# Kernel tuning notes

Measured on AMD Instinct MI355X. Metric: run time of the kernel, lower is better.

Reference implementation:

```python
import jax, jax.numpy as jnp
import numpy as np

L, H, HD, D, FF, V, S_LEN = 12, 12, 64, 768, 3072, 50257, 1024
NEG = jnp.finfo(jnp.float32).min


def _ln(x, g, b, eps=1e-5):
    mu = x.mean(-1, keepdims=True)
    var = ((x - mu) ** 2).mean(-1, keepdims=True)
    return (x - mu) * jax.lax.rsqrt(var + eps) * g + b


def setup_inputs() -> dict:
    key = jax.random.key(0)
    ks = jax.random.split(key, 14)
    n = lambda k, shp, s=0.02: jax.random.normal(k, shp, jnp.float32) * s
    return {
        "input_ids": jax.random.randint(ks[0], (1, S_LEN), 0, V, dtype=jnp.int32),
        "attention_mask": jnp.ones((1, S_LEN), jnp.int32),
        "wte": n(ks[1], (V, D)),
        "wpe": n(ks[2], (S_LEN, D)),
        "ln1_g": 1.0 + n(ks[3], (L, D), 0.01),
        "ln1_b": n(ks[4], (L, D), 0.01),
        "W_qkv": n(ks[5], (L, D, 3 * D)),
        "b_qkv": n(ks[6], (L, 3 * D)),
        "W_o": n(ks[7], (L, D, D)),
        "b_o": n(ks[8], (L, D)),
        "ln2_g": 1.0 + n(ks[9], (L, D), 0.01),
        "ln2_b": n(ks[10], (L, D), 0.01),
        "W_fc": n(ks[11], (L, D, FF)),
        "b_fc": n(ks[12], (L, FF)),
        "W_proj": n(ks[13], (L, FF, D)),
        "b_proj": jnp.zeros((L, D), jnp.float32),
        "S": 20, "Sa1": 21, "S2": 600,
    }


def reference(input_ids, attention_mask, wte, wpe, ln1_g, ln1_b, W_qkv, b_qkv,
              W_o, b_o, ln2_g, ln2_b, W_fc, b_fc, W_proj, b_proj, S, Sa1, S2):
    T = input_ids.shape[-1]
    h0 = wte[input_ids[0]] + wpe[:T]                      # [T, D]
    causal = jnp.tril(jnp.ones((T, T), bool))
    add_mask = (1.0 - attention_mask[0].astype(jnp.float32)) * NEG  # [T]
    scale = 1.0 / np.sqrt(HD).astype(np.float32)

    def step(h, p):
        (l1g, l1b, Wqkv, bqkv, Wo, bo, l2g, l2b, Wfc, bfc, Wp, bp) = p
        xl = _ln(h, l1g, l1b)                             # pre-block LN, [T, D]
        # ---- standard GPT-2 block forward (advances hidden state) ----
        qkv = xl @ Wqkv + bqkv
        q, k, v = jnp.split(qkv, 3, axis=-1)
        q = q.reshape(T, H, HD).transpose(1, 0, 2)        # [H, T, HD]
        k = k.reshape(T, H, HD).transpose(1, 0, 2)
        v = v.reshape(T, H, HD).transpose(1, 0, 2)
        sc = jnp.einsum('hqd,hkd->hqk', q, k) * scale
        sc = jnp.where(causal, sc, NEG) + add_mask
        ctx = jnp.einsum('hqk,hkd->hqd', jax.nn.softmax(sc, axis=-1), v)
        attn_out = ctx.transpose(1, 0, 2).reshape(T, D) @ Wo + bo
        h2 = h + attn_out
        h_new = h2 + (jax.nn.gelu(_ln(h2, l2g, l2b) @ Wfc + bfc,
                                  approximate=True) @ Wp + bp)
        # ---- manual QK circuit decomposition (pre-block hidden state) ----
        Wq, Wk, _ = jnp.split(Wqkv, 3, axis=1)            # [D, D] each
        bq, bk, _ = jnp.split(bqkv, 3, axis=0)            # [D] each
        Wmhq = Wq.reshape(D, H, HD).transpose(1, 0, 2)    # [H, D, HD]
        Wmhk = Wk.reshape(D, H, HD).transpose(1, 0, 2)
        bqh = bq.reshape(H, HD)                           # [H, HD]
        bkh = bk.reshape(H, HD)
        qc = jnp.einsum('td,hdk->htk', xl, Wmhq)          # x W_q per head
        kc = jnp.einsum('td,hdk->htk', xl, Wmhk)          # x W_k per head
        term1 = jnp.einsum('hqk,htk->hqt', qc, kc)                 # x Wq Wk^T x^T
        term2 = jnp.einsum('hk,htk->ht', bqh, kc)[:, None, :]      # bq Wk^T x^T
        term3 = jnp.einsum('hqk,hk->hq', qc, bkh)[:, :, None]      # x Wq bk^T
        term4 = jnp.einsum('hk,hk->h', bqh, bkh)[:, None, None]    # bq bk^T
        scores = (term1 + term2 + term3 + term4) * scale
        aw = jax.nn.softmax(jnp.where(causal, scores, NEG), axis=-1)  # [H, T, T]
        dup = aw[:, S2, S]
        ind = aw[:, S2, Sa1]
        prev = aw[:, -1, S2]
        return h_new, (dup, ind, prev, prev)

    params = (ln1_g, ln1_b, W_qkv, b_qkv, W_o, b_o,
              ln2_g, ln2_b, W_fc, b_fc, W_proj, b_proj)
    _, (dup, ind, prev, name) = jax.lax.scan(step, h0, params)
    return dup, ind, prev, name   # each [L, H] = [12, 12]
```

## Files before the change

kernel.cpp:

```cpp
#include <hip/hip_runtime.h>
#include <hip/hip_bf16.h>
#include <math.h>

namespace {

constexpr int T = 1024;
constexpr int D = 768;
constexpr int FF = 3072;
constexpr int H = 12;
constexpr int HD = 64;
constexpr int L = 12;
constexpr float SCALE = 0.125f;

typedef __attribute__((ext_vector_type(8))) short short8;
typedef __attribute__((ext_vector_type(4))) float floatx4;

__device__ inline unsigned short f2bf(float f) {
    __hip_bfloat16 h = __float2bfloat16(f);
    return *reinterpret_cast<unsigned short*>(&h);
}
__device__ inline float bf2f(unsigned short u) {
    union { unsigned int i; float f; } c;
    c.i = (unsigned int)u << 16;
    return c.f;
}

__global__ void embed_kernel(const int* __restrict__ ids,
                             const float* __restrict__ wte,
                             const float* __restrict__ wpe,
                             float* __restrict__ h) {
    int i = blockIdx.x * blockDim.x + threadIdx.x;
    if (i >= T * D) return;
    int t = i / D, d = i % D;
    h[i] = wte[(long)ids[t] * D + d] + wpe[i];
}

__global__ __launch_bounds__(256)
void ln_kernel(const float* __restrict__ x, const float* __restrict__ g,
               const float* __restrict__ b, unsigned short* __restrict__ out) {
    int row = blockIdx.x, tid = threadIdx.x;
    const float* xr = x + (long)row * D;
    float v0 = xr[tid], v1 = xr[tid + 256], v2 = xr[tid + 512];
    __shared__ float red[4];
    __shared__ float share;
    float s = v0 + v1 + v2;
#pragma unroll
    for (int o = 32; o; o >>= 1) s += __shfl_down(s, o, 64);
    if ((tid & 63) == 0) red[tid >> 6] = s;
    __syncthreads();
    if (tid == 0) share = (red[0] + red[1] + red[2] + red[3]) * (1.0f / D);
    __syncthreads();
    float mu = share;
    float d0 = v0 - mu, d1 = v1 - mu, d2 = v2 - mu;
    float q = d0 * d0 + d1 * d1 + d2 * d2;
#pragma unroll
    for (int o = 32; o; o >>= 1) q += __shfl_down(q, o, 64);
    __syncthreads();
    if ((tid & 63) == 0) red[tid >> 6] = q;
    __syncthreads();
    if (tid == 0) share = rsqrtf((red[0] + red[1] + red[2] + red[3]) * (1.0f / D) + 1e-5f);
    __syncthreads();
    float rs = share;
    unsigned short* orow = out + (long)row * D;
    orow[tid]       = f2bf(d0 * rs * g[tid]       + b[tid]);
    orow[tid + 256] = f2bf(d1 * rs * g[tid + 256] + b[tid + 256]);
    orow[tid + 512] = f2bf(d2 * rs * g[tid + 512] + b[tid + 512]);
}

__global__ __launch_bounds__(256)
void wconvert_b(const float* __restrict__ W, unsigned short* __restrict__ WT,
                int K, int N) {
    const int zl = blockIdx.z;
    W  += (long)zl * K * N;
    WT += (long)zl * N * K;
    __shared__ float t[32][33];
    const int n0 = blockIdx.x * 32, k0 = blockIdx.y * 32;
    const int tx = threadIdx.x, ty = threadIdx.y;
#pragma unroll
    for (int i = 0; i < 4; i++)
        t[ty * 4 + i][tx] = W[(long)(k0 + ty * 4 + i) * N + n0 + tx];
    __syncthreads();
#pragma unroll
    for (int i = 0; i < 4; i++)
        WT[(long)(n0 + ty * 4 + i) * K + k0 + tx] = f2bf(t[tx][ty * 4 + i]);
}

#define GEMM_CORE(KLEN)                                                                 \
    floatx4 acc[2][4] = {};                                                             \
    {                                                                                   \
        *(short8*)&As[0][ablk][sl][0]     = *(const short8*)(ApA);                      \
        *(short8*)&As[0][ablk + 4][sl][0] = *(const short8*)(ApB);                      \
        *(short8*)&Bs[0][ablk][sl][0]     = *(const short8*)(Bp);                       \
    }                                                                                   \
    __syncthreads();                                                                    \
    const int nsteps = (KLEN) >> 5;                                                     \
    for (int s = 0; s < nsteps; s++) {                                                  \
        const int buf = s & 1;                                                          \
        short8 na0, na1, nbv;                                                           \
        const bool has_next = (s + 1 < nsteps);                                         \
        if (has_next) {                                                                 \
            na0 = *(const short8*)(ApA + (s + 1) * 32);                                 \
            na1 = *(const short8*)(ApB + (s + 1) * 32);                                 \
            nbv = *(const short8*)(Bp + (s + 1) * 32);                                  \
        }                                                                               \
        short8 af[2], bfr[4];                                                           \
        _Pragma("unroll")                                                               \
        for (int mi = 0; mi < 2; mi++)                                                  \
            af[mi] = *(const short8*)&As[buf][w * 2 + mi][lane][0];                     \
        _Pragma("unroll")                                                               \
        for (int ni = 0; ni < 4; ni++)                                                  \
            bfr[ni] = *(const short8*)&Bs[buf][ni][lane][0];                            \
        _Pragma("unroll")                                                               \
        for (int mi = 0; mi < 2; mi++)                                                  \
            _Pragma("unroll")                                                           \
            for (int ni = 0; ni < 4; ni++)                                              \
                acc[mi][ni] = __builtin_amdgcn_mfma_f32_16x16x32_bf16(                  \
                    af[mi], bfr[ni], acc[mi][ni], 0, 0, 0);                             \
        if (has_next) {                                                                 \
            const int nb = buf ^ 1;                                                     \
            *(short8*)&As[nb][ablk][sl][0]     = na0;                                   \
            *(short8*)&As[nb][ablk + 4][sl][0] = na1;                                   \
            *(short8*)&Bs[nb][ablk][sl][0]     = nbv;                                   \
        }                                                                               \
        __syncthreads();                                                                \
    }

#define GEMM_PRELUDE(KOFF)                                                              \
    const int tid = threadIdx.x;                                                        \
    const int w = tid >> 6, lane = tid & 63;                                            \
    const int ablk = tid >> 6;                                                          \
    const int sl = tid & 63;                                                            \
    const int row0 = blockIdx.y * 128, col0 = blockIdx.x * 64;                          \
    __shared__ unsigned short As[2][8][64][8];                                          \
    __shared__ unsigned short Bs[2][4][64][8];                                          \
    const unsigned short* ApA = A + (long)(row0 + ablk * 16 + (sl & 15)) * K + (KOFF) + (sl >> 4) * 8; \
    const unsigned short* ApB = ApA + 64L * K;                                          \
    const unsigned short* Bp  = BT + (long)(col0 + ablk * 16 + (sl & 15)) * K + (KOFF) + (sl >> 4) * 8;

__global__ __launch_bounds__(256)
void gemm_fused(const unsigned short* __restrict__ A, const unsigned short* __restrict__ BT,
                const float* __restrict__ bias, unsigned short* __restrict__ Cb,
                int N, int K, int flags) {
    GEMM_PRELUDE(0)
    GEMM_CORE(K)
#pragma unroll
    for (int mi = 0; mi < 2; mi++) {
        int rg = row0 + (w * 2 + mi) * 16 + (lane >> 4) * 4;
#pragma unroll
        for (int ni = 0; ni < 4; ni++) {
            int cg = col0 + ni * 16 + (lane & 15);
            float bv = (flags & 1) ? bias[cg] : 0.f;
            float bscale = ((flags & 16) && cg < D) ? SCALE : 1.0f;
#pragma unroll
            for (int r = 0; r < 4; r++) {
                float v = acc[mi][ni][r] + bv;
                if (flags & 4) {
                    float zz = 0.7978845608028654f * (v + 0.044715f * v * v * v);
                    v = v / (1.0f + __expf(-2.0f * zz));
                }
                Cb[(long)(rg + r) * N + cg] = f2bf(v * bscale);
            }
        }
    }
}

__global__ __launch_bounds__(256)
void gemm_bf16(const unsigned short* __restrict__ A, const unsigned short* __restrict__ BT,
               float* __restrict__ part, int N, int K, int splitK) {
    const int z = blockIdx.z;
    const int Kc = K / splitK;
    GEMM_PRELUDE(z * Kc)
    GEMM_CORE(Kc)
    float* dst = part + (long)z * T * N;
#pragma unroll
    for (int mi = 0; mi < 2; mi++) {
        int rg = row0 + (w * 2 + mi) * 16 + (lane >> 4) * 4;
#pragma unroll
        for (int ni = 0; ni < 4; ni++) {
            int cg = col0 + ni * 16 + (lane & 15);
#pragma unroll
            for (int r = 0; r < 4; r++)
                dst[(long)(rg + r) * N + cg] = acc[mi][ni][r];
        }
    }
}

__global__ __launch_bounds__(256)
void reduce_ln(const float* __restrict__ part, const float* __restrict__ bias,
               const float* __restrict__ resid,
               const float* __restrict__ g, const float* __restrict__ b,
               float* __restrict__ Cres, unsigned short* __restrict__ Cln,
               int splitK) {
    const int row = blockIdx.x, tid = threadIdx.x;
    const int c0 = tid, c1 = tid + 256, c2 = tid + 512;
    const long rb = (long)row * D;
    float v0 = bias[c0] + resid[rb + c0];
    float v1 = bias[c1] + resid[rb + c1];
    float v2 = bias[c2] + resid[rb + c2];
    for (int z = 0; z < splitK; z++) {
        const float* p = part + (long)z * T * D + rb;
        v0 += p[c0]; v1 += p[c1]; v2 += p[c2];
    }
    float* crow = Cres + rb;
    crow[c0] = v0; crow[c1] = v1; crow[c2] = v2;
    __shared__ float red[4];
    __shared__ float share;
    float s = v0 + v1 + v2;
#pragma unroll
    for (int o = 32; o; o >>= 1) s += __shfl_down(s, o, 64);
    if ((tid & 63) == 0) red[tid >> 6] = s;
    __syncthreads();
    if (tid == 0) share = (red[0] + red[1] + red[2] + red[3]) * (1.0f / D);
    __syncthreads();
    float mu = share;
    float d0 = v0 - mu, d1 = v1 - mu, d2 = v2 - mu;
    float q = d0 * d0 + d1 * d1 + d2 * d2;
#pragma unroll
    for (int o = 32; o; o >>= 1) q += __shfl_down(q, o, 64);
    __syncthreads();
    if ((tid & 63) == 0) red[tid >> 6] = q;
    __syncthreads();
    if (tid == 0) share = rsqrtf((red[0] + red[1] + red[2] + red[3]) * (1.0f / D) + 1e-5f);
    __syncthreads();
    float rs = share;
    unsigned short* orow = Cln + rb;
    orow[c0] = f2bf(d0 * rs * g[c0] + b[c0]);
    orow[c1] = f2bf(d1 * rs * g[c1] + b[c1]);
    orow[c2] = f2bf(d2 * rs * g[c2] + b[c2]);
}

__global__ __launch_bounds__(256)
void flash_mfma(const unsigned short* __restrict__ qkvb, unsigned short* __restrict__ ctxb) {
    const int h = blockIdx.y;
    const int q0 = blockIdx.x * 64;
    const int tid = threadIdx.x;
    const int w = tid >> 6;
    const int l = tid & 63;
    const int lm = l & 15;
    const int g = l >> 4;

    __shared__ unsigned short Kl[64][72];
    __shared__ unsigned short Vt[64][80];
    __shared__ unsigned short Pl[4][16][72];

    short8 qf[2];
    {
        const unsigned short* qp = qkvb + (long)(q0 + w * 16 + lm) * (3 * D) + h * HD + g * 8;
        qf[0] = *(const short8*)(qp);
        qf[1] = *(const short8*)(qp + 32);
    }

    const int d8 = (tid & 7) * 8;
    const int kp = (tid >> 3) * 2;

    float m = -INFINITY, lsum = 0.f;
    floatx4 o[4] = {};
    const int qw = q0 + w * 16;
    const int nt = blockIdx.x + 1;

    for (int t = 0; t < nt; t++) {
        const int c0 = t * 64;
        __syncthreads();
        {
            const unsigned short* kr0 = qkvb + (long)(c0 + kp) * (3 * D) + D + h * HD + d8;
            const unsigned short* kr1 = kr0 + 3 * D;
            *(short8*)&Kl[kp][d8]     = *(const short8*)kr0;
            *(short8*)&Kl[kp + 1][d8] = *(const short8*)kr1;
            short8 va = *(const short8*)(kr0 + D);
            short8 vb = *(const short8*)(kr1 + D);
#pragma unroll
            for (int j = 0; j < 8; j++) {
                unsigned int pk = (unsigned)(unsigned short)va[j] |
                                  ((unsigned)(unsigned short)vb[j] << 16);
                *(unsigned int*)&Vt[d8 + j][kp] = pk;
            }
        }
        __syncthreads();

        if (c0 > qw + 15) continue;

        floatx4 st[4] = {};
#pragma unroll
        for (int ks = 0; ks < 2; ks++)
#pragma unroll
            for (int mt = 0; mt < 4; mt++) {
                short8 af = *(const short8*)&Kl[mt * 16 + lm][ks * 32 + g * 8];
                st[mt] = __builtin_amdgcn_mfma_f32_16x16x32_bf16(af, qf[ks], st[mt], 0, 0, 0);
            }

        const int qg = qw + lm;
        if (c0 + 63 > qw) {
#pragma unroll
            for (int mt = 0; mt < 4; mt++)
#pragma unroll
                for (int r = 0; r < 4; r++)
                    if (c0 + mt * 16 + g * 4 + r > qg) st[mt][r] = -INFINITY;
        }
        float tmax = -INFINITY;
#pragma unroll
        for (int mt = 0; mt < 4; mt++)
#pragma unroll
            for (int r = 0; r < 4; r++) tmax = fmaxf(tmax, st[mt][r]);
        tmax = fmaxf(tmax, __shfl_xor(tmax, 16));
        tmax = fmaxf(tmax, __shfl_xor(tmax, 32));
        float mn = fmaxf(m, tmax);
        float alpha = __expf(m - mn);
        float psum = 0.f;
        unsigned short pb[16];
#pragma unroll
        for (int mt = 0; mt < 4; mt++)
#pragma unroll
            for (int r = 0; r < 4; r++) {
                float p = __expf(st[mt][r] - mn);
                psum += p;
                pb[mt * 4 + r] = f2bf(p);
            }
        lsum = lsum * alpha + psum;
        m = mn;
#pragma unroll
        for (int mt = 0; mt < 4; mt++) {
            unsigned int p0 = (unsigned)pb[mt * 4 + 0] | ((unsigned)pb[mt * 4 + 1] << 16);
            unsigned int p1 = (unsigned)pb[mt * 4 + 2] | ((unsigned)pb[mt * 4 + 3] << 16);
            *(unsigned int*)&Pl[w][lm][mt * 16 + g * 4]     = p0;
            *(unsigned int*)&Pl[w][lm][mt * 16 + g * 4 + 2] = p1;
        }
        float ar0 = __shfl(alpha, g * 4 + 0), ar1 = __shfl(alpha, g * 4 + 1);
        float ar2 = __shfl(alpha, g * 4 + 2), ar3 = __shfl(alpha, g * 4 + 3);
#pragma unroll
        for (int fd = 0; fd < 4; fd++) {
            o[fd][0] *= ar0; o[fd][1] *= ar1; o[fd][2] *= ar2; o[fd][3] *= ar3;
        }
#pragma unroll
        for (int ks = 0; ks < 2; ks++) {
            short8 pa = *(const short8*)&Pl[w][lm][ks * 32 + g * 8];
#pragma unroll
            for (int fd = 0; fd < 4; fd++) {
                short8 vb = *(const short8*)&Vt[fd * 16 + lm][ks * 32 + g * 8];
                o[fd] = __builtin_amdgcn_mfma_f32_16x16x32_bf16(pa, vb, o[fd], 0, 0, 0);
            }
        }
    }
    float l2 = lsum + __shfl_xor(lsum, 16);
    float l4 = l2 + __shfl_xor(l2, 32);
    float linv = 1.0f / l4;
    float lr0 = __shfl(linv, g * 4 + 0), lr1 = __shfl(linv, g * 4 + 1);
    float lr2 = __shfl(linv, g * 4 + 2), lr3 = __shfl(linv, g * 4 + 3);
#pragma unroll
    for (int fd = 0; fd < 4; fd++) {
        unsigned short* cp = ctxb + (long)(qw + g * 4) * D + h * HD + fd * 16 + lm;
        cp[0 * D] = f2bf(o[fd][0] * lr0);
        cp[1 * D] = f2bf(o[fd][1] * lr1);
        cp[2 * D] = f2bf(o[fd][2] * lr2);
        cp[3 * D] = f2bf(o[fd][3] * lr3);
    }
}

__global__ __launch_bounds__(256)
void probe_kernel(const unsigned short* __restrict__ qkvb,
                  const int* __restrict__ Sp, const int* __restrict__ Sa1p,
                  const int* __restrict__ S2p,
                  float* __restrict__ out, int layer) {
    const int h = blockIdx.y;
    const int which = blockIdx.x;
    const int s = *Sp, sa1 = *Sa1p, s2 = *S2p;
    const int row = which ? (T - 1) : s2;
    const int tid = threadIdx.x;
    __shared__ float qrow[64];
    __shared__ float prob[T];
    __shared__ float red[4];
    __shared__ float bshare;
    if (tid < 64) qrow[tid] = bf2f(qkvb[(long)row * (3 * D) + h * HD + tid]);
    __syncthreads();
    float mloc = -INFINITY;
    for (int j = tid; j <= row; j += 256) {
        const unsigned short* krow = qkvb + (long)j * (3 * D) + D + h * HD;
        float acc = 0;
#pragma unroll
        for (int d = 0; d < 64; d += 8) {
            short8 kv = *(const short8*)(krow + d);
#pragma unroll
            for (int e = 0; e < 8; e++)
                acc += qrow[d + e] * bf2f((unsigned short)kv[e]);
        }
        prob[j] = acc;
        mloc = fmaxf(mloc, acc);
    }
#pragma unroll
    for (int o = 32; o; o >>= 1) mloc = fmaxf(mloc, __shfl_down(mloc, o, 64));
    if ((tid & 63) == 0) red[tid >> 6] = mloc;
    __syncthreads();
    if (tid == 0) bshare = fmaxf(fmaxf(red[0], red[1]), fmaxf(red[2], red[3]));
    __syncthreads();
    float m = bshare;
    float ssum = 0;
    for (int j = tid; j <= row; j += 256) {
        float e = expf(prob[j] - m);
        prob[j] = e;
        ssum += e;
    }
#pragma unroll
    for (int o = 32; o; o >>= 1) ssum += __shfl_down(ssum, o, 64);
    __syncthreads();
    if ((tid & 63) == 0) red[tid >> 6] = ssum;
    __syncthreads();
    if (tid == 0) bshare = red[0] + red[1] + red[2] + red[3];
    __syncthreads();
    float inv = 1.0f / bshare;
    if (tid == 0) {
        if (which == 0) {
            out[0 * (L * H) + layer * H + h] = prob[s] * inv;
            out[1 * (L * H) + layer * H + h] = prob[sa1] * inv;
        } else {
            out[2 * (L * H) + layer * H + h] = prob[s2] * inv;
            out[3 * (L * H) + layer * H + h] = prob[s2] * inv;
        }
    }
}

}

extern "C" void kernel_launch(void* const* d_in, const int* in_sizes, int n_in,
                              void* d_out, int out_size, void* d_ws, size_t ws_size,
                              hipStream_t stream) {
    const int*   ids    = (const int*)  d_in[0];
    const float* wte    = (const float*)d_in[2];
    const float* wpe    = (const float*)d_in[3];
    const float* ln1_g  = (const float*)d_in[4];
    const float* ln1_b  = (const float*)d_in[5];
    const float* W_qkv  = (const float*)d_in[6];
    const float* b_qkv  = (const float*)d_in[7];
    const float* W_o    = (const float*)d_in[8];
    const float* b_o    = (const float*)d_in[9];
    const float* ln2_g  = (const float*)d_in[10];
    const float* ln2_b  = (const float*)d_in[11];
    const float* W_fc   = (const float*)d_in[12];
    const float* b_fc   = (const float*)d_in[13];
    const float* W_proj = (const float*)d_in[14];
    const float* b_proj = (const float*)d_in[15];
    const int*   Sp     = (const int*)  d_in[16];
    const int*   Sa1p   = (const int*)  d_in[17];
    const int*   S2p    = (const int*)  d_in[18];
    float* out = (float*)d_out;

    float* ws   = (float*)d_ws;
    float* h    = ws;
    float* h2   = h   + (long)T * D;
    float* part = h2  + (long)T * D;
    unsigned short* xl   = (unsigned short*)(part + 4L * T * D);
    unsigned short* qkvb = xl   + (long)T * D;
    unsigned short* ctxb = qkvb + (long)T * 3 * D;
    unsigned short* fb   = ctxb + (long)T * D;
    unsigned short* wt_qkv  = fb      + (long)T * FF;
    unsigned short* wt_o    = wt_qkv  + (long)L * 3 * D * D;
    unsigned short* wt_fc   = wt_o    + (long)L * D * D;
    unsigned short* wt_proj = wt_fc   + (long)L * D * FF;

    embed_kernel<<<(T * D + 255) / 256, 256, 0, stream>>>(ids, wte, wpe, h);
    wconvert_b<<<dim3(3 * D / 32, D / 32, L), dim3(32, 8), 0, stream>>>(W_qkv, wt_qkv, D, 3 * D);
    wconvert_b<<<dim3(D / 32, D / 32, L), dim3(32, 8), 0, stream>>>(W_o, wt_o, D, D);
    wconvert_b<<<dim3(FF / 32, D / 32, L), dim3(32, 8), 0, stream>>>(W_fc, wt_fc, D, FF);
    wconvert_b<<<dim3(D / 32, FF / 32, L), dim3(32, 8), 0, stream>>>(W_proj, wt_proj, FF, D);
    ln_kernel<<<T, 256, 0, stream>>>(h, ln1_g, ln1_b, xl);

    for (int l = 0; l < L; l++) {
        gemm_fused<<<dim3(3 * D / 64, T / 128), 256, 0, stream>>>(
            xl, wt_qkv + (long)l * 3 * D * D, b_qkv + (long)l * 3 * D,
            qkvb, 3 * D, D, 1 | 16);
        probe_kernel<<<dim3(2, H), 256, 0, stream>>>(qkvb, Sp, Sa1p, S2p, out, l);

        if (l == L - 1) break;

        flash_mfma<<<dim3(T / 64, H), 256, 0, stream>>>(qkvb, ctxb);
        gemm_bf16<<<dim3(D / 64, T / 128, 4), 256, 0, stream>>>(
            ctxb, wt_o + (long)l * D * D, part, D, D, 4);
        reduce_ln<<<T, 256, 0, stream>>>(
            part, b_o + (long)l * D, h, ln2_g + l * D, ln2_b + l * D, h2, xl, 4);
        gemm_fused<<<dim3(FF / 64, T / 128), 256, 0, stream>>>(
            xl, wt_fc + (long)l * D * FF, b_fc + (long)l * FF, fb, FF, D, 1 | 4);
        gemm_bf16<<<dim3(D / 64, T / 128, 4), 256, 0, stream>>>(
            fb, wt_proj + (long)l * D * FF, part, D, FF, 4);
        reduce_ln<<<T, 256, 0, stream>>>(
            part, b_proj + (long)l * D, h2, ln1_g + (l + 1) * D, ln1_b + (l + 1) * D, h, xl, 4);
    }
}
```

Baseline: 1.421 ms.

## Split flash attention across two key halves and use direct global-to-LDS GEMM loads

The flash attention kernel now splits each query tile's key range into two halves along a new grid z dimension. Each half writes unnormalized fp32 partial outputs plus its running max and sum, and a new merge kernel combines them into bf16 context. This doubles the block count so the GPU's compute units stay busier, at the cost of an extra kernel launch and extra fp32 traffic. Separately, the GEMM core now loads tiles with global_load_lds, which writes straight into LDS instead of staging through registers. That should cut register pressure and VGPR-to-LDS store instructions.

```diff
diff --git a/kernel.cpp b/kernel.cpp
--- a/kernel.cpp
+++ b/kernel.cpp
@@ -23,6 +23,11 @@
     union { unsigned int i; float f; } c;
     c.i = (unsigned int)u << 16;
     return c.f;
+}
+__device__ inline void gld16(const void* g, void* l) {
+    __builtin_amdgcn_global_load_lds(
+        (const __attribute__((address_space(1))) void*)g,
+        (__attribute__((address_space(3))) void*)l, 16, 0, 0);
 }
 
 __global__ void embed_kernel(const int* __restrict__ ids,
@@ -87,21 +92,18 @@
 
 #define GEMM_CORE(KLEN)                                                                 \
     floatx4 acc[2][4] = {};                                                             \
-    {                                                                                   \
-        *(short8*)&As[0][ablk][sl][0]     = *(const short8*)(ApA);                      \
-        *(short8*)&As[0][ablk + 4][sl][0] = *(const short8*)(ApB);                      \
-        *(short8*)&Bs[0][ablk][sl][0]     = *(const short8*)(Bp);                       \
-    }                                                                                   \
+    gld16(ApA, &As[0][ablk][0][0]);                                                     \
+    gld16(ApB, &As[0][ablk + 4][0][0]);                                                 \
+    gld16(Bp,  &Bs[0][ablk][0][0]);                                                     \
     __syncthreads();                                                                    \
     const int nsteps = (KLEN) >> 5;                                                     \
     for (int s = 0; s < nsteps; s++) {                                                  \
         const int buf = s & 1;                                                          \
-        short8 na0, na1, nbv;                                                           \
-        const bool has_next = (s + 1 < nsteps);                                         \
-        if (has_next) {                                                                 \
-            na0 = *(const short8*)(ApA + (s + 1) * 32);                                 \
-            na1 = *(const short8*)(ApB + (s + 1) * 32);                                 \
-            nbv = *(const short8*)(Bp + (s + 1) * 32);                                  \
+        const int nb = buf ^ 1;                                                         \
+        if (s + 1 < nsteps) {                                                           \
+            gld16(ApA + (s + 1) * 32, &As[nb][ablk][0][0]);                             \
+            gld16(ApB + (s + 1) * 32, &As[nb][ablk + 4][0][0]);                         \
+            gld16(Bp  + (s + 1) * 32, &Bs[nb][ablk][0][0]);                             \
         }                                                                               \
         short8 af[2], bfr[4];                                                           \
         _Pragma("unroll")                                                               \
@@ -116,12 +118,6 @@
             for (int ni = 0; ni < 4; ni++)                                              \
                 acc[mi][ni] = __builtin_amdgcn_mfma_f32_16x16x32_bf16(                  \
                     af[mi], bfr[ni], acc[mi][ni], 0, 0, 0);                             \
-        if (has_next) {                                                                 \
-            const int nb = buf ^ 1;                                                     \
-            *(short8*)&As[nb][ablk][sl][0]     = na0;                                   \
-            *(short8*)&As[nb][ablk + 4][sl][0] = na1;                                   \
-            *(short8*)&Bs[nb][ablk][sl][0]     = nbv;                                   \
-        }                                                                               \
         __syncthreads();                                                                \
     }
 
@@ -230,9 +226,11 @@
 }
 
 __global__ __launch_bounds__(256)
-void flash_mfma(const unsigned short* __restrict__ qkvb, unsigned short* __restrict__ ctxb) {
+void flash_mfma(const unsigned short* __restrict__ qkvb,
+                float* __restrict__ o_part, float2* __restrict__ ml) {
     const int h = blockIdx.y;
     const int q0 = blockIdx.x * 64;
+    const int zsp = blockIdx.z;
     const int tid = threadIdx.x;
     const int w = tid >> 6;
     const int l = tid & 63;
@@ -257,8 +255,11 @@
     floatx4 o[4] = {};
     const int qw = q0 + w * 16;
     const int nt = blockIdx.x + 1;
-
-    for (int t = 0; t < nt; t++) {
+    const int half = (nt + 1) >> 1;
+    const int tbeg = zsp ? half : 0;
+    const int tend = zsp ? nt : half;
+
+    for (int t = tbeg; t < tend; t++) {
         const int c0 = t * 64;
         __syncthreads();
         {
@@ -342,17 +343,37 @@
     }
     float l2 = lsum + __shfl_xor(lsum, 16);
     float l4 = l2 + __shfl_xor(l2, 32);
-    float linv = 1.0f / l4;
-    float lr0 = __shfl(linv, g * 4 + 0), lr1 = __shfl(linv, g * 4 + 1);
-    float lr2 = __shfl(linv, g * 4 + 2), lr3 = __shfl(linv, g * 4 + 3);
+    float* op = o_part + (long)zsp * T * D;
 #pragma unroll
     for (int fd = 0; fd < 4; fd++) {
-        unsigned short* cp = ctxb + (long)(qw + g * 4) * D + h * HD + fd * 16 + lm;
-        cp[0 * D] = f2bf(o[fd][0] * lr0);
-        cp[1 * D] = f2bf(o[fd][1] * lr1);
-        cp[2 * D] = f2bf(o[fd][2] * lr2);
-        cp[3 * D] = f2bf(o[fd][3] * lr3);
-    }
+        float* cp = op + (long)(qw + g * 4) * D + h * HD + fd * 16 + lm;
+        cp[0 * D] = o[fd][0];
+        cp[1 * D] = o[fd][1];
+        cp[2 * D] = o[fd][2];
+        cp[3 * D] = o[fd][3];
+    }
+    if (l < 16) ml[(long)zsp * T * H + (long)(qw + lm) * H + h] = make_float2(m, l4);
+}
+
+__global__ __launch_bounds__(256)
+void merge_flash(const float* __restrict__ o_part, const float2* __restrict__ ml,
+                 unsigned short* __restrict__ ctxb) {
+    long idx = ((long)blockIdx.x * 256 + threadIdx.x) * 4;
+    if (idx >= (long)T * D) return;
+    int q = (int)(idx / D), d = (int)(idx % D);
+    int h = d >> 6;
+    float2 a = ml[(long)q * H + h];
+    float2 b = ml[(long)T * H + (long)q * H + h];
+    float M = fmaxf(a.x, b.x);
+    float e1 = __expf(a.x - M), e2 = __expf(b.x - M);
+    float inv = 1.0f / (a.y * e1 + b.y * e2);
+    float4 o1 = *(const float4*)(o_part + idx);
+    float4 o2 = *(const float4*)(o_part + (long)T * D + idx);
+    unsigned short* dst = ctxb + idx;
+    dst[0] = f2bf((o1.x * e1 + o2.x * e2) * inv);
+    dst[1] = f2bf((o1.y * e1 + o2.y * e2) * inv);
+    dst[2] = f2bf((o1.z * e1 + o2.z * e2) * inv);
+    dst[3] = f2bf((o1.w * e1 + o2.w * e2) * inv);
 }
 
 __global__ __launch_bounds__(256)
@@ -446,6 +467,8 @@
     float* h    = ws;
     float* h2   = h   + (long)T * D;
     float* part = h2  + (long)T * D;
+    float*  o_part = part;
+    float2* mlbuf  = (float2*)(part + 2L * T * D);
     unsigned short* xl   = (unsigned short*)(part + 4L * T * D);
     unsigned short* qkvb = xl   + (long)T * D;
     unsigned short* ctxb = qkvb + (long)T * 3 * D;
@@ -470,7 +493,8 @@
 
         if (l == L - 1) break;
 
-        flash_mfma<<<dim3(T / 64, H), 256, 0, stream>>>(qkvb, ctxb);
+        flash_mfma<<<dim3(T / 64, H, 2), 256, 0, stream>>>(qkvb, o_part, mlbuf);
+        merge_flash<<<(T * D / 4 + 255) / 256, 256, 0, stream>>>(o_part, mlbuf, ctxb);
         gemm_bf16<<<dim3(D / 64, T / 128, 4), 256, 0, stream>>>(
             ctxb, wt_o + (long)l * D * D, part, D, D, 4);
         reduce_ln<<<T, 256, 0, stream>>>(
```

Result: no change. 1.424 ms (+0.2%).

## Use direct global-to-LDS loads in GEMM and fuse probe into flash attention

Applied to the files above, without the earlier changes.

The GEMM staging loop now uses global_load_lds to copy A and B tiles straight into shared memory instead of going through registers with explicit LDS stores. The probe blocks become extra blocks of the flash attention launch, which removes one kernel launch per layer on all but the last layer. Risks: the global_load_lds LDS layout (wave-base pointer plus per-lane 16B offsets) must match the previous per-lane layout. The combined kernel also carries the probe's shared-memory arrays, which may lower occupancy for the flash blocks.

```diff
diff --git a/kernel.cpp b/kernel.cpp
--- a/kernel.cpp
+++ b/kernel.cpp
@@ -23,6 +23,11 @@
     union { unsigned int i; float f; } c;
     c.i = (unsigned int)u << 16;
     return c.f;
+}
+__device__ inline void gld16(const void* g, void* l) {
+    __builtin_amdgcn_global_load_lds(
+        (const __attribute__((address_space(1))) void*)g,
+        (__attribute__((address_space(3))) void*)l, 16, 0, 0);
 }
 
 __global__ void embed_kernel(const int* __restrict__ ids,
@@ -87,21 +92,18 @@
 
 #define GEMM_CORE(KLEN)                                                                 \
     floatx4 acc[2][4] = {};                                                             \
-    {                                                                                   \
-        *(short8*)&As[0][ablk][sl][0]     = *(const short8*)(ApA);                      \
-        *(short8*)&As[0][ablk + 4][sl][0] = *(const short8*)(ApB);                      \
-        *(short8*)&Bs[0][ablk][sl][0]     = *(const short8*)(Bp);                       \
-    }                                                                                   \
+    gld16(ApA, &As[0][ablk][0][0]);                                                     \
+    gld16(ApB, &As[0][ablk + 4][0][0]);                                                 \
+    gld16(Bp,  &Bs[0][ablk][0][0]);                                                     \
     __syncthreads();                                                                    \
     const int nsteps = (KLEN) >> 5;                                                     \
     for (int s = 0; s < nsteps; s++) {                                                  \
         const int buf = s & 1;                                                          \
-        short8 na0, na1, nbv;                                                           \
-        const bool has_next = (s + 1 < nsteps);                                         \
-        if (has_next) {                                                                 \
-            na0 = *(const short8*)(ApA + (s + 1) * 32);                                 \
-            na1 = *(const short8*)(ApB + (s + 1) * 32);                                 \
-            nbv = *(const short8*)(Bp + (s + 1) * 32);                                  \
+        const int nb = buf ^ 1;                                                         \
+        if (s + 1 < nsteps) {                                                           \
+            gld16(ApA + (s + 1) * 32, &As[nb][ablk][0][0]);                             \
+            gld16(ApB + (s + 1) * 32, &As[nb][ablk + 4][0][0]);                         \
+            gld16(Bp  + (s + 1) * 32, &Bs[nb][ablk][0][0]);                             \
         }                                                                               \
         short8 af[2], bfr[4];                                                           \
         _Pragma("unroll")                                                               \
@@ -116,12 +118,6 @@
             for (int ni = 0; ni < 4; ni++)                                              \
                 acc[mi][ni] = __builtin_amdgcn_mfma_f32_16x16x32_bf16(                  \
                     af[mi], bfr[ni], acc[mi][ni], 0, 0, 0);                             \
-        if (has_next) {                                                                 \
-            const int nb = buf ^ 1;                                                     \
-            *(short8*)&As[nb][ablk][sl][0]     = na0;                                   \
-            *(short8*)&As[nb][ablk + 4][sl][0] = na1;                                   \
-            *(short8*)&Bs[nb][ablk][sl][0]     = nbv;                                   \
-        }                                                                               \
         __syncthreads();                                                                \
     }
 
@@ -229,9 +225,82 @@
     orow[c2] = f2bf(d2 * rs * g[c2] + b[c2]);
 }
 
-__global__ __launch_bounds__(256)
-void flash_mfma(const unsigned short* __restrict__ qkvb, unsigned short* __restrict__ ctxb) {
+__device__ void probe_body(const unsigned short* __restrict__ qkvb,
+                           const int* __restrict__ Sp, const int* __restrict__ Sa1p,
+                           const int* __restrict__ S2p,
+                           float* __restrict__ out, int layer, int which, int h) {
+    const int s = *Sp, sa1 = *Sa1p, s2 = *S2p;
+    const int row = which ? (T - 1) : s2;
+    const int tid = threadIdx.x;
+    __shared__ float qrow[64];
+    __shared__ float prob[T];
+    __shared__ float red[4];
+    __shared__ float bshare;
+    if (tid < 64) qrow[tid] = bf2f(qkvb[(long)row * (3 * D) + h * HD + tid]);
+    __syncthreads();
+    float mloc = -INFINITY;
+    for (int j = tid; j <= row; j += 256) {
+        const unsigned short* krow = qkvb + (long)j * (3 * D) + D + h * HD;
+        float acc = 0;
+#pragma unroll
+        for (int d = 0; d < 64; d += 8) {
+            short8 kv = *(const short8*)(krow + d);
+#pragma unroll
+            for (int e = 0; e < 8; e++)
+                acc += qrow[d + e] * bf2f((unsigned short)kv[e]);
+        }
+        prob[j] = acc;
+        mloc = fmaxf(mloc, acc);
+    }
+#pragma unroll
+    for (int o = 32; o; o >>= 1) mloc = fmaxf(mloc, __shfl_down(mloc, o, 64));
+    if ((tid & 63) == 0) red[tid >> 6] = mloc;
+    __syncthreads();
+    if (tid == 0) bshare = fmaxf(fmaxf(red[0], red[1]), fmaxf(red[2], red[3]));
+    __syncthreads();
+    float m = bshare;
+    float ssum = 0;
+    for (int j = tid; j <= row; j += 256) {
+        float e = expf(prob[j] - m);
+        prob[j] = e;
+        ssum += e;
+    }
+#pragma unroll
+    for (int o = 32; o; o >>= 1) ssum += __shfl_down(ssum, o, 64);
+    __syncthreads();
+    if ((tid & 63) == 0) red[tid >> 6] = ssum;
+    __syncthreads();
+    if (tid == 0) bshare = red[0] + red[1] + red[2] + red[3];
+    __syncthreads();
+    float inv = 1.0f / bshare;
+    if (tid == 0) {
+        if (which == 0) {
+            out[0 * (L * H) + layer * H + h] = prob[s] * inv;
+            out[1 * (L * H) + layer * H + h] = prob[sa1] * inv;
+        } else {
+            out[2 * (L * H) + layer * H + h] = prob[s2] * inv;
+            out[3 * (L * H) + layer * H + h] = prob[s2] * inv;
+        }
+    }
+}
+
+__global__ __launch_bounds__(256)
+void probe_kernel(const unsigned short* __restrict__ qkvb,
+                  const int* __restrict__ Sp, const int* __restrict__ Sa1p,
+                  const int* __restrict__ S2p,
+                  float* __restrict__ out, int layer) {
+    probe_body(qkvb, Sp, Sa1p, S2p, out, layer, blockIdx.x, blockIdx.y);
+}
+
+__global__ __launch_bounds__(256)
+void flash_probe(const unsigned short* __restrict__ qkvb, unsigned short* __restrict__ ctxb,
+                 const int* __restrict__ Sp, const int* __restrict__ Sa1p,
+                 const int* __restrict__ S2p, float* __restrict__ out, int layer) {
     const int h = blockIdx.y;
+    if (blockIdx.x >= T / 64) {
+        probe_body(qkvb, Sp, Sa1p, S2p, out, layer, blockIdx.x - T / 64, h);
+        return;
+    }
     const int q0 = blockIdx.x * 64;
     const int tid = threadIdx.x;
     const int w = tid >> 6;
@@ -352,68 +421,6 @@
         cp[1 * D] = f2bf(o[fd][1] * lr1);
         cp[2 * D] = f2bf(o[fd][2] * lr2);
         cp[3 * D] = f2bf(o[fd][3] * lr3);
-    }
-}
-
-__global__ __launch_bounds__(256)
-void probe_kernel(const unsigned short* __restrict__ qkvb,
-                  const int* __restrict__ Sp, const int* __restrict__ Sa1p,
-                  const int* __restrict__ S2p,
-                  float* __restrict__ out, int layer) {
-    const int h = blockIdx.y;
-    const int which = blockIdx.x;
-    const int s = *Sp, sa1 = *Sa1p, s2 = *S2p;
-    const int row = which ? (T - 1) : s2;
-    const int tid = threadIdx.x;
-    __shared__ float qrow[64];
-    __shared__ float prob[T];
-    __shared__ float red[4];
-    __shared__ float bshare;
-    if (tid < 64) qrow[tid] = bf2f(qkvb[(long)row * (3 * D) + h * HD + tid]);
-    __syncthreads();
-    float mloc = -INFINITY;
-    for (int j = tid; j <= row; j += 256) {
-        const unsigned short* krow = qkvb + (long)j * (3 * D) + D + h * HD;
-        float acc = 0;
-#pragma unroll
-        for (int d = 0; d < 64; d += 8) {
-            short8 kv = *(const short8*)(krow + d);
-#pragma unroll
-            for (int e = 0; e < 8; e++)
-                acc += qrow[d + e] * bf2f((unsigned short)kv[e]);
-        }
-        prob[j] = acc;
-        mloc = fmaxf(mloc, acc);
-    }
-#pragma unroll
-    for (int o = 32; o; o >>= 1) mloc = fmaxf(mloc, __shfl_down(mloc, o, 64));
-    if ((tid & 63) == 0) red[tid >> 6] = mloc;
-    __syncthreads();
-    if (tid == 0) bshare = fmaxf(fmaxf(red[0], red[1]), fmaxf(red[2], red[3]));
-    __syncthreads();
-    float m = bshare;
-    float ssum = 0;
-    for (int j = tid; j <= row; j += 256) {
-        float e = expf(prob[j] - m);
-        prob[j] = e;
-        ssum += e;
-    }
-#pragma unroll
-    for (int o = 32; o; o >>= 1) ssum += __shfl_down(ssum, o, 64);
-    __syncthreads();
-    if ((tid & 63) == 0) red[tid >> 6] = ssum;
-    __syncthreads();
-    if (tid == 0) bshare = red[0] + red[1] + red[2] + red[3];
-    __syncthreads();
-    float inv = 1.0f / bshare;
-    if (tid == 0) {
-        if (which == 0) {
-            out[0 * (L * H) + layer * H + h] = prob[s] * inv;
-            out[1 * (L * H) + layer * H + h] = prob[sa1] * inv;
-        } else {
-            out[2 * (L * H) + layer * H + h] = prob[s2] * inv;
-            out[3 * (L * H) + layer * H + h] = prob[s2] * inv;
-        }
     }
 }
 
@@ -466,11 +473,14 @@
         gemm_fused<<<dim3(3 * D / 64, T / 128), 256, 0, stream>>>(
             xl, wt_qkv + (long)l * 3 * D * D, b_qkv + (long)l * 3 * D,
             qkvb, 3 * D, D, 1 | 16);
-        probe_kernel<<<dim3(2, H), 256, 0, stream>>>(qkvb, Sp, Sa1p, S2p, out, l);
-
-        if (l == L - 1) break;
-
-        flash_mfma<<<dim3(T / 64, H), 256, 0, stream>>>(qkvb, ctxb);
+
+        if (l == L - 1) {
+            probe_kernel<<<dim3(2, H), 256, 0, stream>>>(qkvb, Sp, Sa1p, S2p, out, l);
+            break;
+        }
+
+        flash_probe<<<dim3(T / 64 + 2, H), 256, 0, stream>>>(
+            qkvb, ctxb, Sp, Sa1p, S2p, out, l);
         gemm_bf16<<<dim3(D / 64, T / 128, 4), 256, 0, stream>>>(
             ctxb, wt_o + (long)l * D * D, part, D, D, 4);
         reduce_ln<<<T, 256, 0, stream>>>(
```

Measured after the change: 1.357 ms. 4.5% less time.
